# Kernel tuning notes

Measured on AMD Instinct MI355X. Metric: run time of the kernel, lower is better.

## Reference

```python
import jax, jax.numpy as jnp
import numpy as np

# geomloss SamplesLoss('sinkhorn', p=2, blur=0.05, scaling=0.5, debias=True) math
P = 2
BLUR = 0.05
SCALING = 0.5
DIAMETER = 64.0  # static conservative bound on point-cloud diameter for randn D=64 data


def _eps_schedule():
    eps_list = []
    e = DIAMETER ** P
    target = BLUR ** P
    while e > target:
        eps_list.append(e)
        e *= SCALING ** P
    eps_list.append(target)
    return np.array(eps_list, dtype=np.float32)


def _cost(x, y):
    # C_ij = ||x_i - y_j||^2 / 2   (p=2 cost of geomloss)
    sq = (jnp.sum(x * x, -1)[:, :, None] * 0.5
          + jnp.sum(y * y, -1)[:, None, :] * 0.5
          - jnp.einsum('bnd,bmd->bnm', x, y))
    return jnp.maximum(sq, 0.0)


def _softmin(eps, C, h):
    # f_i = -eps * log sum_j exp(h_j - C_ij / eps);  C: (B,N,M), h: (B,M)
    return -eps * jax.nn.logsumexp(h[:, None, :] - C / eps, axis=-1)


def setup_inputs() -> dict:
    key = jax.random.key(0)
    k1, k2, k3, k4 = jax.random.split(key, 4)
    B, N, M, D = 8, 2048, 2048, 64
    x = jax.random.normal(k1, (B, N, D), dtype=jnp.float32)
    y = jax.random.normal(k2, (B, M, D), dtype=jnp.float32)
    w1 = jax.random.uniform(k3, (B, N), dtype=jnp.float32) + 0.01
    w2 = jax.random.uniform(k4, (B, M), dtype=jnp.float32) + 0.01
    w1 = w1 / jnp.sum(w1, axis=-1, keepdims=True)
    w2 = w2 / jnp.sum(w2, axis=-1, keepdims=True)
    return {'x': x, 'y': y, 'w1': w1, 'w2': w2}


def _sinkhorn_divergence(x, y, w1, w2):
    a_log = jnp.log(w1)
    b_log = jnp.log(w2)
    eps_list = jnp.asarray(_eps_schedule())

    # --- Sinkhorn loop on detached quantities (geomloss detaches the loop) ---
    xd = jax.lax.stop_gradient(x)
    yd = jax.lax.stop_gradient(y)
    ald = jax.lax.stop_gradient(a_log)
    bld = jax.lax.stop_gradient(b_log)
    C_xy_d = _cost(xd, yd)
    C_yx_d = jnp.swapaxes(C_xy_d, 1, 2)
    C_xx_d = _cost(xd, xd)
    C_yy_d = _cost(yd, yd)

    eps0 = eps_list[0]
    f_ab = _softmin(eps0, C_xy_d, bld)
    g_ba = _softmin(eps0, C_yx_d, ald)
    f_aa = _softmin(eps0, C_xx_d, ald)
    g_bb = _softmin(eps0, C_yy_d, bld)

    def step(carry, eps):
        f_ab, g_ba, f_aa, g_bb = carry
        ft = _softmin(eps, C_xy_d, bld + g_ba / eps)
        gt = _softmin(eps, C_yx_d, ald + f_ab / eps)
        f_aa_t = _softmin(eps, C_xx_d, ald + f_aa / eps)
        g_bb_t = _softmin(eps, C_yy_d, bld + g_bb / eps)
        return (0.5 * (f_ab + ft), 0.5 * (g_ba + gt),
                0.5 * (f_aa + f_aa_t), 0.5 * (g_bb + g_bb_t)), None

    (f_ab, g_ba, f_aa, g_bb), _ = jax.lax.scan(step, (f_ab, g_ba, f_aa, g_bb), eps_list)

    # --- last extrapolation at eps = blur^p, differentiable ---
    eps = eps_list[-1]
    C_xy = _cost(x, y)
    C_yx = jnp.swapaxes(C_xy, 1, 2)
    C_xx = _cost(x, x)
    C_yy = _cost(y, y)
    f_ab_f = _softmin(eps, C_xy, b_log + g_ba / eps)
    g_ba_f = _softmin(eps, C_yx, a_log + f_ab / eps)
    f_aa_f = _softmin(eps, C_xx, a_log + f_aa / eps)
    g_bb_f = _softmin(eps, C_yy, b_log + g_bb / eps)

    # debiased sinkhorn cost per batch element
    loss = (jnp.sum(w1 * (f_ab_f - f_aa_f), axis=-1)
            + jnp.sum(w2 * (g_ba_f - g_bb_f), axis=-1))
    return loss


def reference(x, y, w1, w2):
    loss = _sinkhorn_divergence(x, y, w1, w2)
    return jnp.mean(loss)  # reduction='mean'
```

## Files before the change

### kernel.cpp

```cpp
#include <hip/hip_runtime.h>

#define NB 8
#define NN 2048
#define MM 2048
#define DD 64
#define NMAT ((size_t)NN * (size_t)MM)
#define NCHK 16
#define TS 128

#define CSCALE 320.0f
#define CDEC   (1.0f / CSCALE)

__device__ unsigned short g_C[3 * NB * NMAT];
__device__ float g_fab[3][NB * NN], g_gba[3][NB * NN];
__device__ float g_faa[3][NB * NN], g_gbb[3][NB * NN];
__device__ float g_alog[NB * NN], g_blog[NB * NN];
__device__ float g_xn[NB * NN], g_yn[NB * NN];
__device__ float g_h0[NB * MM], g_h1[NB * NN], g_h2[NB * NN], g_h3[NB * MM];
__device__ float2 g_pfab[NB * NCHK * NN];
__device__ float2 g_pgba[NB * NCHK * NN];
__device__ float2 g_pfaa[NB * NCHK * NN];
__device__ float2 g_pgbb[NB * NCHK * NN];

__global__ __launch_bounds__(256) void prep_kernel(
    const float* __restrict__ x, const float* __restrict__ y,
    const float* __restrict__ w1, const float* __restrict__ w2)
{
  int gid = blockIdx.x * 256 + threadIdx.x;
  if (gid < NB * NN) {
    g_alog[gid] = logf(w1[gid]);
    g_blog[gid] = logf(w2[gid]);
  }
  int lane = threadIdx.x & 63;
  int row = blockIdx.x * 4 + (threadIdx.x >> 6);
  float xv = x[(size_t)row * DD + lane];
  float yv = y[(size_t)row * DD + lane];
  float sx = xv * xv;
  float sy = yv * yv;
#pragma unroll
  for (int off = 32; off > 0; off >>= 1) {
    sx += __shfl_down(sx, off);
    sy += __shfl_down(sy, off);
  }
  if (lane == 0) {
    g_xn[row] = 0.5f * sx;
    g_yn[row] = 0.5f * sy;
  }
}

__global__ __launch_bounds__(256) void cost_kernel(
    const float* __restrict__ X, const float* __restrict__ Y,
    const float* __restrict__ xn, const float* __restrict__ yn,
    unsigned short* __restrict__ C)
{
  __shared__ float Xs[32 * 128];
  __shared__ float Ys[32 * 128];
  const int b = blockIdx.z;
  const int i0 = blockIdx.y * 128;
  const int j0 = blockIdx.x * 128;
  const int t = threadIdx.x;
  const float* xb = X + (size_t)b * NN * DD;
  const float* yb = Y + (size_t)b * MM * DD;
  const int tx = t & 15, ty = t >> 4;

  float acc[8][8];
#pragma unroll
  for (int r = 0; r < 8; ++r)
#pragma unroll
    for (int c = 0; c < 8; ++c) acc[r][c] = 0.f;

  for (int kk = 0; kk < 64; kk += 32) {
    if (kk) __syncthreads();
#pragma unroll
    for (int p = 0; p < 4; ++p) {
      int f = p * 256 + t;
      int r = f >> 3;
      int k4 = (f & 7) << 2;
      float4 vx = ((const float4*)(xb + (size_t)(i0 + r) * DD))[(kk >> 2) + (f & 7)];
      int rs = r ^ k4;
      Xs[(k4 + 0) * 128 + rs] = vx.x;
      Xs[(k4 + 1) * 128 + rs] = vx.y;
      Xs[(k4 + 2) * 128 + rs] = vx.z;
      Xs[(k4 + 3) * 128 + rs] = vx.w;
      float4 vy = ((const float4*)(yb + (size_t)(j0 + r) * DD))[(kk >> 2) + (f & 7)];
      Ys[(k4 + 0) * 128 + rs] = vy.x;
      Ys[(k4 + 1) * 128 + rs] = vy.y;
      Ys[(k4 + 2) * 128 + rs] = vy.z;
      Ys[(k4 + 3) * 128 + rs] = vy.w;
    }
    __syncthreads();

#pragma unroll 4
    for (int k = 0; k < 32; ++k) {
      int s = k & 28;
      float a[8], bb[8];
      *(float4*)&a[0]  = *(const float4*)&Xs[k * 128 + ((ty * 8) ^ s)];
      *(float4*)&a[4]  = *(const float4*)&Xs[k * 128 + ((ty * 8 + 4) ^ s)];
      *(float4*)&bb[0] = *(const float4*)&Ys[k * 128 + ((tx * 8) ^ s)];
      *(float4*)&bb[4] = *(const float4*)&Ys[k * 128 + ((tx * 8 + 4) ^ s)];
#pragma unroll
      for (int r = 0; r < 8; ++r)
#pragma unroll
        for (int c = 0; c < 8; ++c)
          acc[r][c] = fmaf(a[r], bb[c], acc[r][c]);
    }
  }

  float xr[8], yc[8];
#pragma unroll
  for (int r = 0; r < 8; ++r) xr[r] = xn[b * NN + i0 + ty * 8 + r];
#pragma unroll
  for (int c = 0; c < 8; ++c) yc[c] = yn[b * MM + j0 + tx * 8 + c];

#pragma unroll
  for (int r = 0; r < 8; ++r) {
    unsigned short* crow = C + (size_t)b * NMAT
                         + (size_t)(i0 + ty * 8 + r) * MM + j0 + tx * 8;
    unsigned int u[8];
#pragma unroll
    for (int c = 0; c < 8; ++c) {
      float cv = fmaxf(xr[r] + yc[c] - acc[r][c], 0.f);
      u[c] = __float2uint_rn(fminf(cv * CSCALE, 65535.f));
    }
    uint4 ow;
    ow.x = u[0] | (u[1] << 16);
    ow.y = u[2] | (u[3] << 16);
    ow.z = u[4] | (u[5] << 16);
    ow.w = u[6] | (u[7] << 16);
    *(uint4*)crow = ow;
  }
}

__global__ __launch_bounds__(256) void hprep_kernel(
    const float* __restrict__ fab_in, const float* __restrict__ gba_in,
    const float* __restrict__ faa_in, const float* __restrict__ gbb_in,
    float gs)
{
  int i = blockIdx.x * 256 + threadIdx.x;
  g_h0[i] = fmaf(gs, gba_in[i], g_blog[i]);
  g_h1[i] = fmaf(gs, fab_in[i], g_alog[i]);
  g_h2[i] = fmaf(gs, faa_in[i], g_alog[i]);
  g_h3[i] = fmaf(gs, gbb_in[i], g_blog[i]);
}

struct TileArgs {
  const unsigned short* C;
  const float* hrow;
  const float* hcol;
  float2* prow;
  float2* pcol;
  int sym;
};

__global__ __launch_bounds__(256) void tile_pass(
    TileArgs T0, TileArgs T1, TileArgs T2, float inv_eps)
{
  TileArgs A = (blockIdx.z == 0) ? T0 : (blockIdx.z == 1) ? T1 : T2;
  int I, J;
  if (A.sym) {
    if (blockIdx.x >= 136) return;
    int rem = blockIdx.x, ii = 0;
    while (rem >= NCHK - ii) { rem -= NCHK - ii; ++ii; }
    I = ii; J = ii + rem;
  } else {
    I = blockIdx.x >> 4;
    J = blockIdx.x & 15;
  }
  const int b = blockIdx.y;
  const int t = threadIdx.x;
  const int ctr = t & 15;
  const int rtr = t >> 4;
  const float csneg = -inv_eps * CDEC;

  const unsigned short* Cb = A.C + (size_t)b * NMAT
                           + (size_t)(I * TS) * MM + J * TS;

  float hr[8], hc[8];
  {
    const float* hrp = A.hrow + (size_t)b * MM + J * TS + ctr * 8;
    const float* hcp = A.hcol + (size_t)b * MM + I * TS + rtr * 8;
#pragma unroll
    for (int k = 0; k < 8; ++k) { hr[k] = hrp[k]; hc[k] = hcp[k]; }
  }

  uint4 cu[8];
#pragma unroll
  for (int r8 = 0; r8 < 8; ++r8)
    cu[r8] = *(const uint4*)(Cb + (size_t)(rtr * 8 + r8) * MM + ctr * 8);

  __shared__ float redR[TS][17], redC[TS][17];
  __shared__ float rowM[TS], colM[TS];

  float rm[8], cm[8];
#pragma unroll
  for (int k = 0; k < 8; ++k) { rm[k] = -3.0e38f; cm[k] = -3.0e38f; }
#pragma unroll
  for (int r8 = 0; r8 < 8; ++r8) {
    float base[8];
    base[0] = (float)(cu[r8].x & 0xffff) * csneg;
    base[1] = (float)(cu[r8].x >> 16)    * csneg;
    base[2] = (float)(cu[r8].y & 0xffff) * csneg;
    base[3] = (float)(cu[r8].y >> 16)    * csneg;
    base[4] = (float)(cu[r8].z & 0xffff) * csneg;
    base[5] = (float)(cu[r8].z >> 16)    * csneg;
    base[6] = (float)(cu[r8].w & 0xffff) * csneg;
    base[7] = (float)(cu[r8].w >> 16)    * csneg;
#pragma unroll
    for (int c8 = 0; c8 < 8; ++c8) {
      rm[r8] = fmaxf(rm[r8], hr[c8] + base[c8]);
      cm[c8] = fmaxf(cm[c8], hc[r8] + base[c8]);
    }
  }
#pragma unroll
  for (int r8 = 0; r8 < 8; ++r8) redR[rtr * 8 + r8][ctr] = rm[r8];
#pragma unroll
  for (int c8 = 0; c8 < 8; ++c8) redC[ctr * 8 + c8][rtr] = cm[c8];
  __syncthreads();
  if (t < TS) {
    float m = redR[t][0];
#pragma unroll
    for (int k = 1; k < 16; ++k) m = fmaxf(m, redR[t][k]);
    rowM[t] = m;
  } else {
    int tt = t - TS;
    float m = redC[tt][0];
#pragma unroll
    for (int k = 1; k < 16; ++k) m = fmaxf(m, redC[tt][k]);
    colM[tt] = m;
  }
  __syncthreads();

  float rmv[8], cmv[8];
#pragma unroll
  for (int k = 0; k < 8; ++k) {
    rmv[k] = rowM[rtr * 8 + k];
    cmv[k] = colM[ctr * 8 + k];
  }

  float rs[8], cs[8];
#pragma unroll
  for (int k = 0; k < 8; ++k) { rs[k] = 0.f; cs[k] = 0.f; }
#pragma unroll
  for (int r8 = 0; r8 < 8; ++r8) {
    float base[8];
    base[0] = (float)(cu[r8].x & 0xffff) * csneg;
    base[1] = (float)(cu[r8].x >> 16)    * csneg;
    base[2] = (float)(cu[r8].y & 0xffff) * csneg;
    base[3] = (float)(cu[r8].y >> 16)    * csneg;
    base[4] = (float)(cu[r8].z & 0xffff) * csneg;
    base[5] = (float)(cu[r8].z >> 16)    * csneg;
    base[6] = (float)(cu[r8].w & 0xffff) * csneg;
    base[7] = (float)(cu[r8].w >> 16)    * csneg;
#pragma unroll
    for (int c8 = 0; c8 < 8; ++c8) {
      rs[r8] += __expf(hr[c8] + base[c8] - rmv[r8]);
      cs[c8] += __expf(hc[r8] + base[c8] - cmv[c8]);
    }
  }
#pragma unroll
  for (int r8 = 0; r8 < 8; ++r8) redR[rtr * 8 + r8][ctr] = rs[r8];
#pragma unroll
  for (int c8 = 0; c8 < 8; ++c8) redC[ctr * 8 + c8][rtr] = cs[c8];
  __syncthreads();
  if (t < TS) {
    float s = 0.f;
#pragma unroll
    for (int k = 0; k < 16; ++k) s += redR[t][k];
    A.prow[((size_t)b * NCHK + J) * NN + I * TS + t] = make_float2(rowM[t], s);
  } else {
    int tt = t - TS;
    if (!(A.sym && I == J)) {
      float s = 0.f;
#pragma unroll
      for (int k = 0; k < 16; ++k) s += redC[tt][k];
      A.pcol[((size_t)b * NCHK + I) * NN + J * TS + tt] = make_float2(colM[tt], s);
    }
  }
}

struct MergeArgs {
  const float2* part;
  const float* fold;
  float* fout;
  const float* hbase;
  float* hout;
};

__global__ __launch_bounds__(256) void merge4(
    MergeArgs M0, MergeArgs M1, MergeArgs M2, MergeArgs M3,
    float eps, float alpha, float beta, float nextgs)
{
  MergeArgs A = (blockIdx.z == 0) ? M0 : (blockIdx.z == 1) ? M1
              : (blockIdx.z == 2) ? M2 : M3;
  const int b = blockIdx.y;
  const int i = blockIdx.x * 256 + threadIdx.x;
  float2 p[NCHK];
#pragma unroll
  for (int k = 0; k < NCHK; ++k)
    p[k] = A.part[((size_t)b * NCHK + k) * NN + i];
  float M = p[0].x;
#pragma unroll
  for (int k = 1; k < NCHK; ++k) M = fmaxf(M, p[k].x);
  float S = 0.f;
#pragma unroll
  for (int k = 0; k < NCHK; ++k) S += p[k].y * __expf(p[k].x - M);
  float ft = -eps * (M + __logf(S));
  int idx = b * NN + i;
  float fnew = alpha * A.fold[idx] + beta * ft;
  A.fout[idx] = fnew;
  A.hout[idx] = fmaf(nextgs, fnew, A.hbase[idx]);
}

__global__ __launch_bounds__(256) void loss_kernel(
    const float* __restrict__ w1, const float* __restrict__ w2,
    float* __restrict__ out)
{
  __shared__ float red[256];
  float acc = 0.f;
  for (int idx = threadIdx.x; idx < NB * NN; idx += 256) {
    acc += w1[idx] * (g_fab[2][idx] - g_faa[2][idx])
         + w2[idx] * (g_gba[2][idx] - g_gbb[2][idx]);
  }
  red[threadIdx.x] = acc;
  __syncthreads();
  for (int s = 128; s > 0; s >>= 1) {
    if (threadIdx.x < s) red[threadIdx.x] += red[threadIdx.x + s];
    __syncthreads();
  }
  if (threadIdx.x == 0) out[0] = red[0] * (1.0f / NB);
}

extern "C" void kernel_launch(void* const* d_in, const int* in_sizes, int n_in,
                              void* d_out, int out_size, void* d_ws, size_t ws_size,
                              hipStream_t stream)
{
  const float* x = (const float*)d_in[0];
  const float* y = (const float*)d_in[1];
  const float* w1 = (const float*)d_in[2];
  const float* w2 = (const float*)d_in[3];
  float* out = (float*)d_out;

  unsigned short* Cbase;
  hipGetSymbolAddress((void**)&Cbase, HIP_SYMBOL(g_C));
  unsigned short* Cxy = Cbase + 0ull * NB * NMAT;
  unsigned short* Cxx = Cbase + 1ull * NB * NMAT;
  unsigned short* Cyy = Cbase + 2ull * NB * NMAT;
  float *xn, *yn, *h0, *h1, *h2, *h3, *fabp, *gbap, *faap, *gbbp, *alog, *blog;
  float2 *pfab, *pgba, *pfaa, *pgbb;
  hipGetSymbolAddress((void**)&xn, HIP_SYMBOL(g_xn));
  hipGetSymbolAddress((void**)&yn, HIP_SYMBOL(g_yn));
  hipGetSymbolAddress((void**)&h0, HIP_SYMBOL(g_h0));
  hipGetSymbolAddress((void**)&h1, HIP_SYMBOL(g_h1));
  hipGetSymbolAddress((void**)&h2, HIP_SYMBOL(g_h2));
  hipGetSymbolAddress((void**)&h3, HIP_SYMBOL(g_h3));
  hipGetSymbolAddress((void**)&fabp, HIP_SYMBOL(g_fab));
  hipGetSymbolAddress((void**)&gbap, HIP_SYMBOL(g_gba));
  hipGetSymbolAddress((void**)&faap, HIP_SYMBOL(g_faa));
  hipGetSymbolAddress((void**)&gbbp, HIP_SYMBOL(g_gbb));
  hipGetSymbolAddress((void**)&alog, HIP_SYMBOL(g_alog));
  hipGetSymbolAddress((void**)&blog, HIP_SYMBOL(g_blog));
  hipGetSymbolAddress((void**)&pfab, HIP_SYMBOL(g_pfab));
  hipGetSymbolAddress((void**)&pgba, HIP_SYMBOL(g_pgba));
  hipGetSymbolAddress((void**)&pfaa, HIP_SYMBOL(g_pfaa));
  hipGetSymbolAddress((void**)&pgbb, HIP_SYMBOL(g_pgbb));

  auto fab = [&](int s) { return fabp + (size_t)s * NB * NN; };
  auto gba = [&](int s) { return gbap + (size_t)s * NB * NN; };
  auto faa = [&](int s) { return faap + (size_t)s * NB * NN; };
  auto gbb = [&](int s) { return gbbp + (size_t)s * NB * NN; };

  float eps_list[32];
  int ne = 0;
  {
    double v = 64.0 * 64.0;
    double tgt = 0.05 * 0.05;
    while (v > tgt) { eps_list[ne++] = (float)v; v *= 0.25; }
    eps_list[ne++] = (float)tgt;
  }

  prep_kernel<<<4096, 256, 0, stream>>>(x, y, w1, w2);

  dim3 gg(MM / 128, NN / 128, NB);
  cost_kernel<<<gg, 256, 0, stream>>>(x, y, xn, yn, Cxy);
  cost_kernel<<<gg, 256, 0, stream>>>(x, x, xn, xn, Cxx);
  cost_kernel<<<gg, 256, 0, stream>>>(y, y, yn, yn, Cyy);

  dim3 tg(256, NB, 3);
  dim3 mg(NN / 256, NB, 4);

  auto launch_iter = [&](float eps, float alpha, float beta, float nextgs,
                         int in, int outsel) {
    float inv = 1.0f / eps;
    TileArgs T0 = {Cxy, h0, h1, pfab, pgba, 0};
    TileArgs T1 = {Cxx, h2, h2, pfaa, pfaa, 1};
    TileArgs T2 = {Cyy, h3, h3, pgbb, pgbb, 1};
    tile_pass<<<tg, 256, 0, stream>>>(T0, T1, T2, inv);
    MergeArgs M0 = {pfab, fab(in), fab(outsel), alog, h1};
    MergeArgs M1 = {pgba, gba(in), gba(outsel), blog, h0};
    MergeArgs M2 = {pfaa, faa(in), faa(outsel), alog, h2};
    MergeArgs M3 = {pgbb, gbb(in), gbb(outsel), blog, h3};
    merge4<<<mg, 256, 0, stream>>>(M0, M1, M2, M3, eps, alpha, beta, nextgs);
  };

  hprep_kernel<<<64, 256, 0, stream>>>(fab(0), gba(0), faa(0), gbb(0), 0.f);
  launch_iter(eps_list[0], 0.f, 1.f, 1.0f / eps_list[0], 0, 0);

  int cur = 0;
  for (int k = 0; k < ne; ++k) {
    int nxt = 1 - cur;
    float nextgs = 1.0f / ((k < ne - 1) ? eps_list[k + 1] : eps_list[ne - 1]);
    launch_iter(eps_list[k], 0.5f, 0.5f, nextgs, cur, nxt);
    cur = nxt;
  }

  launch_iter(eps_list[ne - 1], 0.f, 1.f, 0.f, cur, 2);

  loss_kernel<<<1, 256, 0, stream>>>(w1, w2, out);
}
```

Before: 818.8 us.

## Compute cost matrices with fp16 MFMA in one fused launch

The prep kernel now also writes fp16 copies of x and y. The three fp32 SIMT cost GEMMs are replaced by one `cost_mfma` launch that uses 16x16x32 f16 MFMA over 64x64 tiles, covering all three matrices through the z dimension. For the symmetric Cxx and Cyy slabs it skips block tiles below the diagonal at 128 granularity, which presumes the later passes only read the upper half. Each tile is staged in shared memory so global writes are coalesced, at the cost of fp16 rounding error in the dot products that then feeds exp(-C/eps) at small eps.

```diff
diff --git a/kernel.cpp b/kernel.cpp
--- a/kernel.cpp
+++ b/kernel.cpp
@@ -11,7 +11,13 @@
 #define CSCALE 320.0f
 #define CDEC   (1.0f / CSCALE)
 
+typedef _Float16 half_t;
+typedef __attribute__((ext_vector_type(8))) _Float16 f16x8;
+typedef __attribute__((ext_vector_type(4))) float f32x4;
+
 __device__ unsigned short g_C[3 * NB * NMAT];
+__device__ half_t g_xh[NB * NN * DD];
+__device__ half_t g_yh[NB * MM * DD];
 __device__ float g_fab[3][NB * NN], g_gba[3][NB * NN];
 __device__ float g_faa[3][NB * NN], g_gbb[3][NB * NN];
 __device__ float g_alog[NB * NN], g_blog[NB * NN];
@@ -35,6 +41,8 @@
   int row = blockIdx.x * 4 + (threadIdx.x >> 6);
   float xv = x[(size_t)row * DD + lane];
   float yv = y[(size_t)row * DD + lane];
+  g_xh[(size_t)row * DD + lane] = (half_t)xv;
+  g_yh[(size_t)row * DD + lane] = (half_t)yv;
   float sx = xv * xv;
   float sy = yv * yv;
 #pragma unroll
@@ -48,86 +56,63 @@
   }
 }
 
-__global__ __launch_bounds__(256) void cost_kernel(
-    const float* __restrict__ X, const float* __restrict__ Y,
-    const float* __restrict__ xn, const float* __restrict__ yn,
-    unsigned short* __restrict__ C)
-{
-  __shared__ float Xs[32 * 128];
-  __shared__ float Ys[32 * 128];
-  const int b = blockIdx.z;
-  const int i0 = blockIdx.y * 128;
-  const int j0 = blockIdx.x * 128;
+__global__ __launch_bounds__(256) void cost_mfma()
+{
+  const int slab = blockIdx.z >> 3;
+  const int b = blockIdx.z & 7;
+  const int bi = blockIdx.y, bj = blockIdx.x;
+  if (slab && ((bj >> 1) < (bi >> 1))) return;
+
+  const half_t* Ah = (slab == 2) ? g_yh : g_xh;
+  const half_t* Bh = (slab == 0) ? g_yh : ((slab == 1) ? g_xh : g_yh);
+  const float* na = (slab == 2) ? g_yn : g_xn;
+  const float* nbp = (slab == 0) ? g_yn : ((slab == 1) ? g_xn : g_yn);
+  unsigned short* Cout = g_C + (size_t)slab * NB * NMAT + (size_t)b * NMAT;
+
   const int t = threadIdx.x;
-  const float* xb = X + (size_t)b * NN * DD;
-  const float* yb = Y + (size_t)b * MM * DD;
-  const int tx = t & 15, ty = t >> 4;
-
-  float acc[8][8];
-#pragma unroll
-  for (int r = 0; r < 8; ++r)
-#pragma unroll
-    for (int c = 0; c < 8; ++c) acc[r][c] = 0.f;
-
-  for (int kk = 0; kk < 64; kk += 32) {
-    if (kk) __syncthreads();
-#pragma unroll
-    for (int p = 0; p < 4; ++p) {
-      int f = p * 256 + t;
-      int r = f >> 3;
-      int k4 = (f & 7) << 2;
-      float4 vx = ((const float4*)(xb + (size_t)(i0 + r) * DD))[(kk >> 2) + (f & 7)];
-      int rs = r ^ k4;
-      Xs[(k4 + 0) * 128 + rs] = vx.x;
-      Xs[(k4 + 1) * 128 + rs] = vx.y;
-      Xs[(k4 + 2) * 128 + rs] = vx.z;
-      Xs[(k4 + 3) * 128 + rs] = vx.w;
-      float4 vy = ((const float4*)(yb + (size_t)(j0 + r) * DD))[(kk >> 2) + (f & 7)];
-      Ys[(k4 + 0) * 128 + rs] = vy.x;
-      Ys[(k4 + 1) * 128 + rs] = vy.y;
-      Ys[(k4 + 2) * 128 + rs] = vy.z;
-      Ys[(k4 + 3) * 128 + rs] = vy.w;
-    }
-    __syncthreads();
-
-#pragma unroll 4
-    for (int k = 0; k < 32; ++k) {
-      int s = k & 28;
-      float a[8], bb[8];
-      *(float4*)&a[0]  = *(const float4*)&Xs[k * 128 + ((ty * 8) ^ s)];
-      *(float4*)&a[4]  = *(const float4*)&Xs[k * 128 + ((ty * 8 + 4) ^ s)];
-      *(float4*)&bb[0] = *(const float4*)&Ys[k * 128 + ((tx * 8) ^ s)];
-      *(float4*)&bb[4] = *(const float4*)&Ys[k * 128 + ((tx * 8 + 4) ^ s)];
-#pragma unroll
-      for (int r = 0; r < 8; ++r)
-#pragma unroll
-        for (int c = 0; c < 8; ++c)
-          acc[r][c] = fmaf(a[r], bb[c], acc[r][c]);
-    }
-  }
-
-  float xr[8], yc[8];
-#pragma unroll
-  for (int r = 0; r < 8; ++r) xr[r] = xn[b * NN + i0 + ty * 8 + r];
-#pragma unroll
-  for (int c = 0; c < 8; ++c) yc[c] = yn[b * MM + j0 + tx * 8 + c];
-
-#pragma unroll
-  for (int r = 0; r < 8; ++r) {
-    unsigned short* crow = C + (size_t)b * NMAT
-                         + (size_t)(i0 + ty * 8 + r) * MM + j0 + tx * 8;
-    unsigned int u[8];
-#pragma unroll
-    for (int c = 0; c < 8; ++c) {
-      float cv = fmaxf(xr[r] + yc[c] - acc[r][c], 0.f);
-      u[c] = __float2uint_rn(fminf(cv * CSCALE, 65535.f));
-    }
-    uint4 ow;
-    ow.x = u[0] | (u[1] << 16);
-    ow.y = u[2] | (u[3] << 16);
-    ow.z = u[4] | (u[5] << 16);
-    ow.w = u[6] | (u[7] << 16);
-    *(uint4*)crow = ow;
+  const int w = t >> 6, lane = t & 63;
+  const int m = lane & 15, quad = lane >> 4;
+  const int i0 = bi * 64, j0 = bj * 64;
+
+  const half_t* Ab = Ah + ((size_t)b * NN + i0 + 16 * w + m) * DD + quad * 8;
+  const half_t* Bb = Bh + ((size_t)b * MM + j0 + m) * DD + quad * 8;
+
+  f32x4 acc[4];
+#pragma unroll
+  for (int c = 0; c < 4; ++c) acc[c] = (f32x4){0.f, 0.f, 0.f, 0.f};
+
+#pragma unroll
+  for (int s = 0; s < 2; ++s) {
+    f16x8 a = *(const f16x8*)(Ab + s * 32);
+#pragma unroll
+    for (int c = 0; c < 4; ++c) {
+      f16x8 bf = *(const f16x8*)(Bb + (size_t)(16 * c) * DD + s * 32);
+      acc[c] = __builtin_amdgcn_mfma_f32_16x16x32_f16(a, bf, acc[c], 0, 0, 0);
+    }
+  }
+
+  __shared__ unsigned short tile[64 * 64];
+  float xr[4];
+#pragma unroll
+  for (int r = 0; r < 4; ++r) xr[r] = na[b * NN + i0 + 16 * w + quad * 4 + r];
+#pragma unroll
+  for (int c = 0; c < 4; ++c) {
+    float yv = nbp[b * MM + j0 + 16 * c + m];
+#pragma unroll
+    for (int r = 0; r < 4; ++r) {
+      float cv = fmaxf(xr[r] + yv - acc[c][r], 0.f);
+      unsigned int u = __float2uint_rn(fminf(cv * CSCALE, 65535.f));
+      tile[(16 * w + quad * 4 + r) * 64 + 16 * c + m] = (unsigned short)u;
+    }
+  }
+  __syncthreads();
+
+  const uint4* tl = (const uint4*)tile;
+#pragma unroll
+  for (int p = 0; p < 2; ++p) {
+    int u = p * 256 + t;
+    int row = u >> 3, c8 = (u & 7) * 8;
+    *(uint4*)(Cout + (size_t)(i0 + row) * MM + j0 + c8) = tl[u];
   }
 }
 
@@ -345,10 +330,8 @@
   unsigned short* Cxy = Cbase + 0ull * NB * NMAT;
   unsigned short* Cxx = Cbase + 1ull * NB * NMAT;
   unsigned short* Cyy = Cbase + 2ull * NB * NMAT;
-  float *xn, *yn, *h0, *h1, *h2, *h3, *fabp, *gbap, *faap, *gbbp, *alog, *blog;
+  float *h0, *h1, *h2, *h3, *fabp, *gbap, *faap, *gbbp, *alog, *blog;
   float2 *pfab, *pgba, *pfaa, *pgbb;
-  hipGetSymbolAddress((void**)&xn, HIP_SYMBOL(g_xn));
-  hipGetSymbolAddress((void**)&yn, HIP_SYMBOL(g_yn));
   hipGetSymbolAddress((void**)&h0, HIP_SYMBOL(g_h0));
   hipGetSymbolAddress((void**)&h1, HIP_SYMBOL(g_h1));
   hipGetSymbolAddress((void**)&h2, HIP_SYMBOL(g_h2));
@@ -380,10 +363,7 @@
 
   prep_kernel<<<4096, 256, 0, stream>>>(x, y, w1, w2);
 
-  dim3 gg(MM / 128, NN / 128, NB);
-  cost_kernel<<<gg, 256, 0, stream>>>(x, y, xn, yn, Cxy);
-  cost_kernel<<<gg, 256, 0, stream>>>(x, x, xn, xn, Cxx);
-  cost_kernel<<<gg, 256, 0, stream>>>(y, y, yn, yn, Cyy);
+  cost_mfma<<<dim3(32, 32, 24), 256, 0, stream>>>();
 
   dim3 tg(256, NB, 3);
   dim3 mg(NN / 256, NB, 4);
```

After: 765.0 us. -6.6%, faster.
